# Kernel tuning notes

Measured on AMD Instinct MI355X. Metric: run time of the kernel, lower is better.

## Reference

```python
import jax, jax.numpy as jnp
import numpy as np

H = 16
D_MODEL = 1024
D_K = D_MODEL // H
NEG = -1e9


def setup_inputs() -> dict:
    key = jax.random.key(0)
    ks = jax.random.split(key, 12)
    B, S = 2, 2048
    inp = {
        "query": jax.random.normal(ks[0], (B, S, D_MODEL), jnp.float32),
        "key": jax.random.normal(ks[1], (B, S, D_MODEL), jnp.float32),
        "value": jax.random.normal(ks[2], (B, S, D_MODEL), jnp.float32),
        "mask": jnp.ones((B, 1, S), jnp.int32),
    }
    s = 1.0 / np.sqrt(D_MODEL)
    for i, nm in enumerate(["Wq", "Wk", "Wv", "Wo"]):
        inp[nm] = jax.random.normal(ks[3 + i], (D_MODEL, D_MODEL), jnp.float32) * s
        inp["b" + nm[1]] = jax.random.normal(ks[7 + i], (D_MODEL,), jnp.float32) * s
    return inp


def _split_heads(x):
    B, S, _ = x.shape
    return x.reshape(B, S, H, D_K).transpose(0, 2, 1, 3)  # [B,H,S,Dk]


def reference(query, key, value, mask, Wq, bq, Wk, bk, Wv, bv, Wo, bo):
    q = _split_heads(query @ Wq + bq)
    k = _split_heads(key @ Wk + bk)
    v = _split_heads(value @ Wv + bv)
    scores = jnp.einsum("bhqd,bhkd->bhqk", q, k) / jnp.sqrt(jnp.float32(D_K))
    # mask [B,1,Sk] -> broadcast as [B,1,1,Sk]
    scores = jnp.where(mask[:, None, :, :] == 0, NEG, scores)
    attn = jax.nn.softmax(scores, axis=-1)  # dropout is identity in eval mode
    out = jnp.einsum("bhqk,bhkd->bhqd", attn, v)
    B, _, Sq, _ = out.shape
    out = out.transpose(0, 2, 1, 3).reshape(B, Sq, H * D_K)
    return out @ Wo + bo
```

## Files before the change

### kernel.cpp

```cpp
#include <hip/hip_runtime.h>
#include <hip/hip_bf16.h>

typedef __attribute__((ext_vector_type(8))) short short8;
typedef __attribute__((ext_vector_type(4))) float float4v;
typedef __attribute__((ext_vector_type(2))) unsigned int uint2v;
typedef __hip_bfloat16 bf16;

#define MFMA16(a, b, c) __builtin_amdgcn_mfma_f32_16x16x32_bf16((a), (b), (c), 0, 0, 0)

static __device__ __forceinline__ short8 load8(const bf16* p) {
    return *reinterpret_cast<const short8*>(p);
}
static __device__ __forceinline__ unsigned short bfu(float x) {
    union { bf16 b; unsigned short u; } c; c.b = __float2bfloat16(x); return c.u;
}
static __device__ __forceinline__ unsigned pack2(float lo, float hi) {
    return ((unsigned)bfu(hi) << 16) | bfu(lo);
}
static __device__ __forceinline__ short bf_bits(float x) {
    union { bf16 b; short u; } c; c.b = __float2bfloat16(x); return c.u;
}
static __device__ __forceinline__ short8 cvt8(float4 a, float4 b) {
    short8 r;
    r[0] = bf_bits(a.x); r[1] = bf_bits(a.y); r[2] = bf_bits(a.z); r[3] = bf_bits(a.w);
    r[4] = bf_bits(b.x); r[5] = bf_bits(b.y); r[6] = bf_bits(b.z); r[7] = bf_bits(b.w);
    return r;
}

typedef const __attribute__((address_space(1))) unsigned int* gp1;
typedef __attribute__((address_space(3))) unsigned int* lp3;
static __device__ __forceinline__ void async16(const void* g, void* l) {
    __builtin_amdgcn_global_load_lds((gp1)g, (lp3)l, 16, 0, 0);
}

__global__ __launch_bounds__(256) void transpose_qkv(
    const float* __restrict__ Wq, const float* __restrict__ Wk,
    const float* __restrict__ Wv, bf16* __restrict__ out_base)
{
    __shared__ bf16 tile[64][65];
    const float* in = (blockIdx.z == 0) ? Wq : (blockIdx.z == 1) ? Wk : Wv;
    bf16* out = out_base + (size_t)blockIdx.z * 1048576;
    int tx = threadIdx.x, ty = threadIdx.y;
    int bx = blockIdx.x * 64, by = blockIdx.y * 64;
    for (int i = ty; i < 64; i += 4)
        tile[i][tx] = __float2bfloat16(in[(size_t)(by + i) * 1024 + bx + tx]);
    __syncthreads();
    for (int i = ty; i < 64; i += 4)
        out[(size_t)(bx + i) * 1024 + by + tx] = tile[tx][i];
}

__global__ __launch_bounds__(256) void transpose_one(
    const float* __restrict__ in, bf16* __restrict__ out)
{
    __shared__ bf16 tile[64][65];
    int tx = threadIdx.x, ty = threadIdx.y;
    int bx = blockIdx.x * 64, by = blockIdx.y * 64;
    for (int i = ty; i < 64; i += 4)
        tile[i][tx] = __float2bfloat16(in[(size_t)(by + i) * 1024 + bx + tx]);
    __syncthreads();
    for (int i = ty; i < 64; i += 4)
        out[(size_t)(bx + i) * 1024 + by + tx] = tile[tx][i];
}

__global__ __launch_bounds__(256, 3) void qkv_gemm(
    const float* __restrict__ Xq, const float* __restrict__ Xk,
    const float* __restrict__ Xv, const bf16* __restrict__ Wt_all,
    const float* __restrict__ bq, const float* __restrict__ bk,
    const float* __restrict__ bv,
    bf16* __restrict__ outq, bf16* __restrict__ outk, bf16* __restrict__ outv)
{
    __shared__ bf16 Bs[2][128 * 64];

    int wg = blockIdx.x;
    int xcd = wg & 7;
    int jj = wg >> 3;
    int grp = xcd * 12 + (jj >> 3);
    int z = grp >> 5;
    int m_blk = grp & 31;
    int n_blk = jj & 7;

    const float* X    = (z == 0) ? Xq : (z == 1) ? Xk : Xv;
    const float* bias = (z == 0) ? bq : (z == 1) ? bk : bv;
    const bf16*  Wt   = Wt_all + (size_t)z * 1048576;
    bf16*        out  = (z == 0) ? outq : (z == 1) ? outk : outv;
    bool vmode = (z == 2);

    int tid = threadIdx.x;
    int w = tid >> 6, lane = tid & 63, l16 = lane & 15, quad = lane >> 4;
    int m_base = m_blk * 128, n_base = n_blk * 128;

    int r8 = lane >> 3, s8 = lane & 7;
    const bf16* Bsrc = Wt + (size_t)(n_base + w * 32 + r8) * 1024 + ((s8 ^ r8) << 3);

    int wm = (w & 1) * 64, wn = (w >> 1) * 64;
    int sw = l16 & 7;

    const float* Abase = X + (size_t)(m_base + wm + l16) * 1024 + quad * 8;

    float4v zero = {0.f, 0.f, 0.f, 0.f};
    float4v acc[4][4];
    #pragma unroll
    for (int mi = 0; mi < 4; ++mi)
        #pragma unroll
        for (int nj = 0; nj < 4; ++nj) acc[mi][nj] = zero;

    #pragma unroll
    for (int p = 0; p < 4; ++p)
        async16(Bsrc + (size_t)p * 8192, (char*)&Bs[0][0] + (w * 32 + p * 8) * 128);
    __syncthreads();

    for (int it = 0; it < 16; ++it) {
        int cur = it & 1;
        int kt = it * 64;
        if (it != 15) {
            #pragma unroll
            for (int p = 0; p < 4; ++p)
                async16(Bsrc + (size_t)p * 8192 + kt + 64,
                        (char*)&Bs[cur ^ 1][0] + (w * 32 + p * 8) * 128);
        }

        const bf16* Bb = &Bs[cur][0];
        #pragma unroll
        for (int kk = 0; kk < 2; ++kk) {
            short8 bfr[4];
            #pragma unroll
            for (int nj = 0; nj < 4; ++nj) {
                const bf16* rp = Bb + (wn + nj * 16 + l16) * 64;
                bfr[nj] = load8(rp + (((kk * 4 + quad) ^ sw) << 3));
            }
            #pragma unroll
            for (int mi = 0; mi < 4; ++mi) {
                const float* ap = Abase + (size_t)mi * 16384 + kt + kk * 32;
                float4 f0 = *(const float4*)(ap);
                float4 f1 = *(const float4*)(ap + 4);
                short8 af = cvt8(f0, f1);
                #pragma unroll
                for (int nj = 0; nj < 4; ++nj)
                    acc[mi][nj] = MFMA16(af, bfr[nj], acc[mi][nj]);
            }
        }
        __syncthreads();
    }

    float bsv[4];
    #pragma unroll
    for (int nj = 0; nj < 4; ++nj)
        bsv[nj] = bias[n_base + wn + nj * 16 + l16];

    #pragma unroll
    for (int mi = 0; mi < 4; ++mi) {
        #pragma unroll
        for (int nj = 0; nj < 4; ++nj) {
            int n = n_base + wn + nj * 16 + l16;
            int h = n >> 6, dk = n & 63;
            int m0 = m_base + wm + mi * 16 + quad * 4;
            int b = m0 >> 11, s0 = m0 & 2047;
            if (vmode) {
                float v0 = acc[mi][nj][0] + bsv[nj];
                float v1 = acc[mi][nj][1] + bsv[nj];
                float v2 = acc[mi][nj][2] + bsv[nj];
                float v3 = acc[mi][nj][3] + bsv[nj];
                uint2 pv; pv.x = pack2(v0, v1); pv.y = pack2(v2, v3);
                size_t idx = ((size_t)(b * 16 + h) * 64 + dk) * 2048 + s0;
                *reinterpret_cast<uint2*>(out + idx) = pv;
            } else {
                #pragma unroll
                for (int r = 0; r < 4; ++r) {
                    size_t idx = (((size_t)(b * 16 + h) * 2048 + s0 + r) * 64 + dk);
                    out[idx] = __float2bfloat16(acc[mi][nj][r] + bsv[nj]);
                }
            }
        }
    }
}

__global__ __launch_bounds__(256, 2) void out_gemm(
    const bf16* __restrict__ A, const bf16* __restrict__ Wt,
    const float* __restrict__ bias, float* __restrict__ out)
{
    __shared__ bf16 As[128 * 128];
    __shared__ bf16 Bs[64 * 128];

    int wg = blockIdx.x;
    int xcd = wg & 7;
    int jj = wg >> 3;
    int m_blk = xcd * 4 + (jj >> 4);
    int n_blk = jj & 15;

    int tid = threadIdx.x;
    int w = tid >> 6, lane = tid & 63, l16 = lane & 15, quad = lane >> 4;
    int m_base = m_blk * 128, n_base = n_blk * 64;

    int r4 = lane >> 4, s16 = lane & 15;

    int wm = (w & 1) * 64, wn = (w >> 1) * 32;

    float4v zero = {0.f, 0.f, 0.f, 0.f};
    float4v acc[4][2];
    #pragma unroll
    for (int mi = 0; mi < 4; ++mi)
        #pragma unroll
        for (int nj = 0; nj < 2; ++nj) acc[mi][nj] = zero;

    for (int it = 0; it < 8; ++it) {
        int kt = it * 128;
        #pragma unroll
        for (int p = 0; p < 8; ++p) {
            int row = w * 32 + p * 4 + r4;
            const bf16* s = A + (size_t)(m_base + row) * 1024 + kt
                              + ((s16 ^ (row & 15)) << 3);
            async16(s, (char*)As + (w * 32 + p * 4) * 256);
        }
        #pragma unroll
        for (int p = 0; p < 4; ++p) {
            int row = w * 16 + p * 4 + r4;
            const bf16* s = Wt + (size_t)(n_base + row) * 1024 + kt
                              + ((s16 ^ (row & 15)) << 3);
            async16(s, (char*)Bs + (w * 16 + p * 4) * 256);
        }
        __syncthreads();

        #pragma unroll
        for (int kk = 0; kk < 4; ++kk) {
            short8 af[4], bfr[2];
            #pragma unroll
            for (int mi = 0; mi < 4; ++mi) {
                const bf16* rp = As + (wm + mi * 16 + l16) * 128;
                af[mi] = load8(rp + (((kk * 4 + quad) ^ l16) << 3));
            }
            #pragma unroll
            for (int nj = 0; nj < 2; ++nj) {
                const bf16* rp = Bs + (wn + nj * 16 + l16) * 128;
                bfr[nj] = load8(rp + (((kk * 4 + quad) ^ l16) << 3));
            }
            #pragma unroll
            for (int mi = 0; mi < 4; ++mi)
                #pragma unroll
                for (int nj = 0; nj < 2; ++nj)
                    acc[mi][nj] = MFMA16(af[mi], bfr[nj], acc[mi][nj]);
        }
        __syncthreads();
    }

    float bsv[2];
    #pragma unroll
    for (int nj = 0; nj < 2; ++nj)
        bsv[nj] = bias[n_base + wn + nj * 16 + l16];

    #pragma unroll
    for (int mi = 0; mi < 4; ++mi)
        #pragma unroll
        for (int nj = 0; nj < 2; ++nj) {
            int n = n_base + wn + nj * 16 + l16;
            int m0 = m_base + wm + mi * 16 + quad * 4;
            #pragma unroll
            for (int r = 0; r < 4; ++r)
                out[(size_t)(m0 + r) * 1024 + n] = acc[mi][nj][r] + bsv[nj];
        }
}

__global__ __launch_bounds__(256, 4) void attn_fused(
    const bf16* __restrict__ Qm, const bf16* __restrict__ Km,
    const bf16* __restrict__ Vt, const int* __restrict__ mask,
    bf16* __restrict__ Oout)
{
    __shared__ __align__(16) bf16 Kc[2][64 * 64];
    __shared__ __align__(16) bf16 Vc[2][64 * 64];
    __shared__ unsigned long long maskb[32];

    int tid = threadIdx.x;
    int w = tid >> 6, lane = tid & 63, l16 = lane & 15, quad = lane >> 4;
    int wg = blockIdx.x;
    int xcd = wg & 7;
    int jj = wg >> 3;
    int bh = xcd * 4 + (jj >> 5);
    int qg = jj & 31;
    int b = bh >> 4, h = bh & 15;
    int qt = qg * 4 + w;

    const int* mb = mask + b * 2048;
    #pragma unroll
    for (int i = 0; i < 8; ++i) {
        unsigned long long bal = __ballot(mb[w * 512 + i * 64 + lane] != 0);
        if (lane == 0) maskb[w * 8 + i] = bal;
    }

    const bf16* Qb = Qm + ((size_t)bh * 2048 + (size_t)qt * 16) * 64;
    short8 bQ0 = load8(Qb + l16 * 64 + quad * 8);
    short8 bQ1 = load8(Qb + l16 * 64 + 32 + quad * 8);

    int r8 = lane >> 3, s8 = lane & 7;
    const bf16* Ksrc = Km + (size_t)bh * 131072 + (size_t)(w * 16 + r8) * 64 + ((s8 ^ r8) << 3);
    const bf16* Vsrc = Vt + (size_t)bh * 131072 + (size_t)(w * 16 + r8) * 2048 + ((s8 ^ r8) << 3);

    int sw = l16 & 7;

    float4v zero = {0.f, 0.f, 0.f, 0.f};
    float4v Oacc[4];
    #pragma unroll
    for (int g = 0; g < 4; ++g) Oacc[g] = zero;
    float lsum = 0.f;
    const float C = 0.18033688f;

    #pragma unroll
    for (int p = 0; p < 2; ++p) {
        async16(Ksrc + (size_t)p * 512,        (char*)&Kc[0][0] + (w * 16 + p * 8) * 128);
        async16(Vsrc + (size_t)p * 8 * 2048,   (char*)&Vc[0][0] + (w * 16 + p * 8) * 128);
    }
    __syncthreads();

    #pragma unroll 2
    for (int it = 0; it < 32; ++it) {
        int cur = it & 1;
        if (it != 31) {
            #pragma unroll
            for (int p = 0; p < 2; ++p) {
                async16(Ksrc + (size_t)(it + 1) * 4096 + p * 512,
                        (char*)&Kc[cur ^ 1][0] + (w * 16 + p * 8) * 128);
                async16(Vsrc + (size_t)(it + 1) * 64 + (size_t)p * 8 * 2048,
                        (char*)&Vc[cur ^ 1][0] + (w * 16 + p * 8) * 128);
            }
        }

        unsigned long long m64 = maskb[it];
        bool full = (m64 == ~0ull);
        const bf16* Kb = &Kc[cur][0];
        const bf16* Vb = &Vc[cur][0];

        float4v S[4];
        #pragma unroll
        for (int kj = 0; kj < 4; ++kj) {
            const bf16* kr = Kb + (kj * 16 + l16) * 64;
            short8 a0 = load8(kr + (((0 + quad) ^ sw) << 3));
            short8 a1 = load8(kr + (((4 + quad) ^ sw) << 3));
            float4v s = MFMA16(a0, bQ0, zero);
            s = MFMA16(a1, bQ1, s);
            S[kj] = s;
        }

        unsigned wlo[4], whi[4];
        #pragma unroll
        for (int kj = 0; kj < 4; ++kj) {
            unsigned m4 = (unsigned)(m64 >> (kj * 16 + quad * 4)) & 0xFu;
            float p[4];
            #pragma unroll
            for (int r = 0; r < 4; ++r)
                p[r] = __builtin_amdgcn_exp2f(S[kj][r] * C);
            if (!full) {
                #pragma unroll
                for (int r = 0; r < 4; ++r)
                    p[r] = ((m4 >> r) & 1u) ? p[r] : 0.f;
            }
            lsum += (p[0] + p[1]) + (p[2] + p[3]);
            wlo[kj] = pack2(p[0], p[1]);
            whi[kj] = pack2(p[2], p[3]);
        }

        short8 ap[2];
        #pragma unroll
        for (int m = 0; m < 2; ++m) {
            uint2v sa = __builtin_amdgcn_permlane32_swap(wlo[2 * m], wlo[2 * m + 1], false, false);
            uint2v qa = __builtin_amdgcn_permlane16_swap(sa[0], sa[1], false, false);
            uint2v sb = __builtin_amdgcn_permlane32_swap(whi[2 * m], whi[2 * m + 1], false, false);
            uint2v qb = __builtin_amdgcn_permlane16_swap(sb[0], sb[1], false, false);
            union { short8 s; unsigned u[4]; } t;
            t.u[0] = qa[0];
            t.u[1] = qb[0];
            t.u[2] = qa[1];
            t.u[3] = qb[1];
            ap[m] = t.s;
        }

        #pragma unroll
        for (int g = 0; g < 4; ++g) {
            const bf16* vr = Vb + (g * 16 + l16) * 64;
            short8 v0 = load8(vr + (((0 + quad) ^ sw) << 3));
            short8 v1 = load8(vr + (((4 + quad) ^ sw) << 3));
            Oacc[g] = MFMA16(ap[0], v0, Oacc[g]);
            Oacc[g] = MFMA16(ap[1], v1, Oacc[g]);
        }

        __syncthreads();
    }

    float ls = lsum;
    ls += __shfl_xor(ls, 16, 64);
    ls += __shfl_xor(ls, 32, 64);
    #pragma unroll
    for (int r = 0; r < 4; ++r) {
        float linv = 1.f / __shfl(ls, quad * 4 + r, 64);
        int srow = qt * 16 + quad * 4 + r;
        size_t base = ((size_t)b * 2048 + srow) * 1024 + h * 64;
        #pragma unroll
        for (int g = 0; g < 4; ++g)
            Oout[base + g * 16 + l16] = __float2bfloat16(Oacc[g][r] * linv);
    }
}

extern "C" void kernel_launch(void* const* d_in, const int* in_sizes, int n_in,
                              void* d_out, int out_size, void* d_ws, size_t ws_size,
                              hipStream_t stream) {
    const float* query = (const float*)d_in[0];
    const float* key   = (const float*)d_in[1];
    const float* value = (const float*)d_in[2];
    const int*   mask  = (const int*)d_in[3];
    const float* Wq = (const float*)d_in[4];
    const float* bq = (const float*)d_in[5];
    const float* Wk = (const float*)d_in[6];
    const float* bk = (const float*)d_in[7];
    const float* Wv = (const float*)d_in[8];
    const float* bv = (const float*)d_in[9];
    const float* Wo = (const float*)d_in[10];
    const float* bo = (const float*)d_in[11];

    char* ws = (char*)d_ws;
    const size_t MB = 1024 * 1024;
    bf16* vb     = (bf16*)ws;
    bf16* Wt_all = (bf16*)(ws + 8 * MB);
    bf16* aout   = (bf16*)(ws + 8 * MB);
    bf16* WtO    = (bf16*)ws;
    bf16* qb     = (bf16*)d_out;
    bf16* kb     = (bf16*)((char*)d_out + 8 * MB);
    float* out   = (float*)d_out;

    transpose_qkv<<<dim3(16, 16, 3), dim3(64, 4), 0, stream>>>(Wq, Wk, Wv, Wt_all);

    qkv_gemm<<<dim3(768), 256, 0, stream>>>(
        query, key, value, Wt_all, bq, bk, bv, qb, kb, vb);

    attn_fused<<<dim3(1024), 256, 0, stream>>>(qb, kb, vb, mask, aout);

    transpose_one<<<dim3(16, 16), dim3(64, 4), 0, stream>>>(Wo, WtO);

    out_gemm<<<dim3(512), 256, 0, stream>>>(aout, WtO, bo, out);
}
```

Before: 287.1 us.

## Stage fp32 activations in LDS for QKV GEMM and widen output GEMM tiles

In the QKV projection, the fp32 activation tile is now copied into shared memory with async loads and an XOR swizzle, replacing direct per-lane global float4 loads. The B tile loses its double buffer and becomes single-buffered, so each iteration loads and then waits on a sync. The output projection GEMM goes from 128x64 to 128x128 tiles, halving the grid to 256 blocks and doubling accumulators per wave to improve operand reuse. The risks are more LDS use, no compute/load overlap in the QKV kernel, and lower occupancy or fewer blocks than CUs in the output GEMM.

```diff
diff --git a/kernel.cpp b/kernel.cpp
--- a/kernel.cpp
+++ b/kernel.cpp
@@ -69,7 +69,8 @@
     const float* __restrict__ bv,
     bf16* __restrict__ outq, bf16* __restrict__ outk, bf16* __restrict__ outv)
 {
-    __shared__ bf16 Bs[2][128 * 64];
+    __shared__ float As[128 * 64];
+    __shared__ bf16  Bs[128 * 64];
 
     int wg = blockIdx.x;
     int xcd = wg & 7;
@@ -89,14 +90,15 @@
     int w = tid >> 6, lane = tid & 63, l16 = lane & 15, quad = lane >> 4;
     int m_base = m_blk * 128, n_base = n_blk * 128;
 
+    int r4 = lane >> 4, s16 = lane & 15;
     int r8 = lane >> 3, s8 = lane & 7;
-    const bf16* Bsrc = Wt + (size_t)(n_base + w * 32 + r8) * 1024 + ((s8 ^ r8) << 3);
+    const float* Asrc0 = X + (size_t)(m_base + w * 32 + r4) * 1024 + ((s16 ^ r4) << 2);
+    const float* Asrc1 = X + (size_t)(m_base + w * 32 + r4) * 1024 + ((s16 ^ (4 + r4)) << 2);
+    const bf16*  Bsrc  = Wt + (size_t)(n_base + w * 32 + r8) * 1024 + ((s8 ^ r8) << 3);
 
     int wm = (w & 1) * 64, wn = (w >> 1) * 64;
     int sw = l16 & 7;
 
-    const float* Abase = X + (size_t)(m_base + wm + l16) * 1024 + quad * 8;
-
     float4v zero = {0.f, 0.f, 0.f, 0.f};
     float4v acc[4][4];
     #pragma unroll
@@ -104,40 +106,38 @@
         #pragma unroll
         for (int nj = 0; nj < 4; ++nj) acc[mi][nj] = zero;
 
-    #pragma unroll
-    for (int p = 0; p < 4; ++p)
-        async16(Bsrc + (size_t)p * 8192, (char*)&Bs[0][0] + (w * 32 + p * 8) * 128);
-    __syncthreads();
-
     for (int it = 0; it < 16; ++it) {
-        int cur = it & 1;
         int kt = it * 64;
-        if (it != 15) {
-            #pragma unroll
-            for (int p = 0; p < 4; ++p)
-                async16(Bsrc + (size_t)p * 8192 + kt + 64,
-                        (char*)&Bs[cur ^ 1][0] + (w * 32 + p * 8) * 128);
-        }
-
-        const bf16* Bb = &Bs[cur][0];
+        #pragma unroll
+        for (int p = 0; p < 8; ++p) {
+            const float* s = ((p & 1) ? Asrc1 : Asrc0) + (size_t)p * 4096 + kt;
+            async16(s, (char*)As + (w * 32 + p * 4) * 256);
+        }
+        #pragma unroll
+        for (int p = 0; p < 4; ++p)
+            async16(Bsrc + (size_t)p * 8192 + kt, (char*)Bs + (w * 32 + p * 8) * 128);
+        __syncthreads();
+
         #pragma unroll
         for (int kk = 0; kk < 2; ++kk) {
-            short8 bfr[4];
+            short8 af[4], bfr[4];
+            #pragma unroll
+            for (int mi = 0; mi < 4; ++mi) {
+                const float* rp = As + (wm + mi * 16 + l16) * 64;
+                float4 f0 = *(const float4*)(rp + (((kk * 8 + quad * 2)     ^ sw) << 2));
+                float4 f1 = *(const float4*)(rp + (((kk * 8 + quad * 2 + 1) ^ sw) << 2));
+                af[mi] = cvt8(f0, f1);
+            }
             #pragma unroll
             for (int nj = 0; nj < 4; ++nj) {
-                const bf16* rp = Bb + (wn + nj * 16 + l16) * 64;
+                const bf16* rp = Bs + (wn + nj * 16 + l16) * 64;
                 bfr[nj] = load8(rp + (((kk * 4 + quad) ^ sw) << 3));
             }
             #pragma unroll
-            for (int mi = 0; mi < 4; ++mi) {
-                const float* ap = Abase + (size_t)mi * 16384 + kt + kk * 32;
-                float4 f0 = *(const float4*)(ap);
-                float4 f1 = *(const float4*)(ap + 4);
-                short8 af = cvt8(f0, f1);
+            for (int mi = 0; mi < 4; ++mi)
                 #pragma unroll
                 for (int nj = 0; nj < 4; ++nj)
-                    acc[mi][nj] = MFMA16(af, bfr[nj], acc[mi][nj]);
-            }
+                    acc[mi][nj] = MFMA16(af[mi], bfr[nj], acc[mi][nj]);
         }
         __syncthreads();
     }
@@ -179,28 +179,28 @@
     const float* __restrict__ bias, float* __restrict__ out)
 {
     __shared__ bf16 As[128 * 128];
-    __shared__ bf16 Bs[64 * 128];
+    __shared__ bf16 Bs[128 * 128];
 
     int wg = blockIdx.x;
     int xcd = wg & 7;
     int jj = wg >> 3;
-    int m_blk = xcd * 4 + (jj >> 4);
-    int n_blk = jj & 15;
+    int m_blk = xcd * 4 + (jj >> 3);
+    int n_blk = jj & 7;
 
     int tid = threadIdx.x;
     int w = tid >> 6, lane = tid & 63, l16 = lane & 15, quad = lane >> 4;
-    int m_base = m_blk * 128, n_base = n_blk * 64;
+    int m_base = m_blk * 128, n_base = n_blk * 128;
 
     int r4 = lane >> 4, s16 = lane & 15;
 
-    int wm = (w & 1) * 64, wn = (w >> 1) * 32;
+    int wm = (w & 1) * 64, wn = (w >> 1) * 64;
 
     float4v zero = {0.f, 0.f, 0.f, 0.f};
-    float4v acc[4][2];
+    float4v acc[4][4];
     #pragma unroll
     for (int mi = 0; mi < 4; ++mi)
         #pragma unroll
-        for (int nj = 0; nj < 2; ++nj) acc[mi][nj] = zero;
+        for (int nj = 0; nj < 4; ++nj) acc[mi][nj] = zero;
 
     for (int it = 0; it < 8; ++it) {
         int kt = it * 128;
@@ -212,45 +212,45 @@
             async16(s, (char*)As + (w * 32 + p * 4) * 256);
         }
         #pragma unroll
-        for (int p = 0; p < 4; ++p) {
-            int row = w * 16 + p * 4 + r4;
+        for (int p = 0; p < 8; ++p) {
+            int row = w * 32 + p * 4 + r4;
             const bf16* s = Wt + (size_t)(n_base + row) * 1024 + kt
                               + ((s16 ^ (row & 15)) << 3);
-            async16(s, (char*)Bs + (w * 16 + p * 4) * 256);
+            async16(s, (char*)Bs + (w * 32 + p * 4) * 256);
         }
         __syncthreads();
 
         #pragma unroll
         for (int kk = 0; kk < 4; ++kk) {
-            short8 af[4], bfr[2];
+            short8 af[4], bfr[4];
             #pragma unroll
             for (int mi = 0; mi < 4; ++mi) {
                 const bf16* rp = As + (wm + mi * 16 + l16) * 128;
                 af[mi] = load8(rp + (((kk * 4 + quad) ^ l16) << 3));
             }
             #pragma unroll
-            for (int nj = 0; nj < 2; ++nj) {
+            for (int nj = 0; nj < 4; ++nj) {
                 const bf16* rp = Bs + (wn + nj * 16 + l16) * 128;
                 bfr[nj] = load8(rp + (((kk * 4 + quad) ^ l16) << 3));
             }
             #pragma unroll
             for (int mi = 0; mi < 4; ++mi)
                 #pragma unroll
-                for (int nj = 0; nj < 2; ++nj)
+                for (int nj = 0; nj < 4; ++nj)
                     acc[mi][nj] = MFMA16(af[mi], bfr[nj], acc[mi][nj]);
         }
         __syncthreads();
     }
 
-    float bsv[2];
-    #pragma unroll
-    for (int nj = 0; nj < 2; ++nj)
+    float bsv[4];
+    #pragma unroll
+    for (int nj = 0; nj < 4; ++nj)
         bsv[nj] = bias[n_base + wn + nj * 16 + l16];
 
     #pragma unroll
     for (int mi = 0; mi < 4; ++mi)
         #pragma unroll
-        for (int nj = 0; nj < 2; ++nj) {
+        for (int nj = 0; nj < 4; ++nj) {
             int n = n_base + wn + nj * 16 + l16;
             int m0 = m_base + wm + mi * 16 + quad * 4;
             #pragma unroll
@@ -432,5 +432,5 @@
 
     transpose_one<<<dim3(16, 16), dim3(64, 4), 0, stream>>>(Wo, WtO);
 
-    out_gemm<<<dim3(512), 256, 0, stream>>>(aout, WtO, bo, out);
-}
+    out_gemm<<<dim3(256), 256, 0, stream>>>(aout, WtO, bo, out);
+}
```

New measurement: 246.9 us. -14.0%, faster.
